# Kernel optimization log

Measured on AMD Instinct MI355X. Metric: run time of the kernel, lower is better.

Reference implementation:

```python
import jax, jax.numpy as jnp
import numpy as np

B, T, X_DIM, H, Y_DIM = 64, 2048, 256, 512, 1

def _lstm_dir(x, lens, w_ih, w_hh, b_ih, b_hh, reverse):
    # x: [B, T, In]; lens: [B] int; w_ih: [4H, In]; w_hh: [4H, H]
    Bb, Tt, _ = x.shape
    Hh = w_hh.shape[-1]
    t_idx = jnp.arange(Tt)
    if reverse:
        # reverse each sequence within its valid length (pack semantics)
        ridx = jnp.clip(lens[:, None] - 1 - t_idx[None, :], 0, Tt - 1)  # [B, T]
        x = jnp.take_along_axis(x, ridx[:, :, None], axis=1)
    valid = (t_idx[None, :] < lens[:, None]).T            # [T, B]
    xT = jnp.swapaxes(x, 0, 1)                            # [T, B, In]
    # hoist the input projection out of the scan (one big GEMM)
    x_proj = jnp.einsum('tbi,gi->tbg', xT, w_ih) + b_ih + b_hh  # [T, B, 4H]
    h0 = jnp.zeros((Bb, Hh), x.dtype)
    c0 = jnp.zeros((Bb, Hh), x.dtype)

    def step(carry, inp):
        h, c = carry
        xp, m = inp                                       # [B,4H], [B]
        g = xp + h @ w_hh.T
        i, f, gg, o = jnp.split(g, 4, axis=-1)            # torch gate order i,f,g,o
        i = jax.nn.sigmoid(i); f = jax.nn.sigmoid(f)
        gg = jnp.tanh(gg); o = jax.nn.sigmoid(o)
        c_new = f * c + i * gg
        h_new = o * jnp.tanh(c_new)
        m = m[:, None]
        h = jnp.where(m, h_new, h)                        # freeze state past seq end
        c = jnp.where(m, c_new, c)
        return (h, c), h

    (h_last, _), outs = jax.lax.scan(step, (h0, c0), (x_proj, valid))
    outs = jnp.swapaxes(outs, 0, 1)                       # [B, T, H]
    if reverse:
        ridx = jnp.clip(lens[:, None] - 1 - t_idx[None, :], 0, Tt - 1)
        outs = jnp.take_along_axis(outs, ridx[:, :, None], axis=1)
    return outs, h_last


def setup_inputs() -> dict:
    key = jax.random.key(0)
    ks = jax.random.split(key, 12)
    s = 1.0 / np.sqrt(H)
    u = lambda k, shp: jax.random.uniform(k, shp, jnp.float32, -s, s)
    seqs = jax.random.normal(ks[0], (B, T, X_DIM), jnp.float32)
    lens = jax.random.randint(ks[1], (B,), 1, T + 1)
    seqs_len = jnp.sort(lens)[::-1].astype(jnp.int64)     # descending, as pack_padded requires
    return {
        'seqs': seqs, 'seqs_len': seqs_len,
        'w_ih_l0': u(ks[2], (2, 4 * H, X_DIM)),   # [dir, 4H, in]
        'w_hh_l0': u(ks[3], (2, 4 * H, H)),
        'b_ih_l0': u(ks[4], (2, 4 * H)),
        'b_hh_l0': u(ks[5], (2, 4 * H)),
        'w_ih_l1': u(ks[6], (2, 4 * H, 2 * H)),
        'w_hh_l1': u(ks[7], (2, 4 * H, H)),
        'b_ih_l1': u(ks[8], (2, 4 * H)),
        'b_hh_l1': u(ks[9], (2, 4 * H)),
        'w_out': u(ks[10], (Y_DIM, 2 * H)),
        'b_out': u(ks[11], (Y_DIM,)),
    }


def reference(seqs, seqs_len, w_ih_l0, w_hh_l0, b_ih_l0, b_hh_l0,
              w_ih_l1, w_hh_l1, b_ih_l1, b_hh_l1, w_out, b_out):
    lens = seqs_len.astype(jnp.int32)
    x = seqs
    h_f = h_b = None
    for (wi, wh, bi, bh) in ((w_ih_l0, w_hh_l0, b_ih_l0, b_hh_l0),
                             (w_ih_l1, w_hh_l1, b_ih_l1, b_hh_l1)):
        out_f, h_f = _lstm_dir(x, lens, wi[0], wh[0], bi[0], bh[0], reverse=False)
        out_b, h_b = _lstm_dir(x, lens, wi[1], wh[1], bi[1], bh[1], reverse=True)
        x = jnp.concatenate([out_f, out_b], axis=-1)      # [B, T, 2H]
    out = jnp.concatenate([h_f, h_b], axis=1)             # last-layer final hidden, [B, 2H]
    out = jax.nn.sigmoid(out @ w_out.T + b_out)           # [B, y_dim]
    return out.squeeze(-1)                                # [B]
```

## Files before the change

### kernel.cpp

```cpp
#include <hip/hip_runtime.h>
#include <stdint.h>
#include <stddef.h>

#define B_  64
#define T_  2048
#define XD  256
#define H_  512
#define G4  2048
#define BT_ (B_*T_)

typedef __attribute__((ext_vector_type(8))) _Float16 f16x8;
typedef __attribute__((ext_vector_type(4))) float f32x4;
typedef __attribute__((ext_vector_type(4))) unsigned int u32x4;
typedef __attribute__((ext_vector_type(4))) unsigned short us4;
typedef __attribute__((ext_vector_type(2))) _Float16 f16x2;

__device__ __attribute__((aligned(256))) unsigned short g_xh[(size_t)BT_*XD];
__device__ __attribute__((aligned(256))) unsigned short g_w1h[(size_t)2*G4*XD];
__device__ __attribute__((aligned(256))) unsigned short g_w2h[(size_t)2*G4*1024];
__device__ __attribute__((aligned(256))) _Float16       g_xproj[(size_t)2*BT_*G4];
__device__ __attribute__((aligned(256))) unsigned short g_out1[(size_t)BT_*1024];
__device__ __attribute__((aligned(256))) unsigned short g_hbuf[2][2][2][B_*H_];
__device__ __attribute__((aligned(256))) float          g_hlast[2][B_*H_];
__device__ __attribute__((aligned(256))) unsigned int   g_flag[2][2][64][64];

__device__ inline unsigned short f2h(float f) {
  _Float16 h = (_Float16)f;
  return __builtin_bit_cast(unsigned short, h);
}
__device__ inline float sigf(float x)  { return 1.f/(1.f + __expf(-x)); }
__device__ inline float tanh_(float x) { return 1.f - 2.f/(__expf(2.f*x) + 1.f); }

__global__ void k_init() {
  unsigned int i = blockIdx.x*256u + threadIdx.x;
  unsigned int stride = gridDim.x*256u;
  unsigned int* hb = (unsigned int*)&g_hbuf[0][0][0][0];
  for (unsigned int j = i; j < sizeof(g_hbuf)/4; j += stride) hb[j] = 0u;
  unsigned int* fl = (unsigned int*)&g_flag[0][0][0][0];
  for (unsigned int j = i; j < sizeof(g_flag)/4; j += stride) fl[j] = 0u;
}

__global__ void k_cvt_x(const float* __restrict__ src) {
  const size_t n4 = (size_t)BT_*XD/4;
  for (size_t j = (size_t)blockIdx.x*blockDim.x + threadIdx.x; j < n4;
       j += (size_t)gridDim.x*blockDim.x) {
    float4 v = ((const float4*)src)[j];
    us4 o = { f2h(v.x), f2h(v.y), f2h(v.z), f2h(v.w) };
    ((us4*)g_xh)[j] = o;
  }
}
__global__ void k_cvt_w1(const float* __restrict__ src) {
  const size_t n4 = (size_t)2*G4*XD/4;
  for (size_t j = (size_t)blockIdx.x*blockDim.x + threadIdx.x; j < n4;
       j += (size_t)gridDim.x*blockDim.x) {
    float4 v = ((const float4*)src)[j];
    us4 o = { f2h(v.x), f2h(v.y), f2h(v.z), f2h(v.w) };
    ((us4*)g_w1h)[j] = o;
  }
}
__global__ void k_cvt_w2(const float* __restrict__ src) {
  const size_t n4 = (size_t)2*G4*1024/4;
  for (size_t j = (size_t)blockIdx.x*blockDim.x + threadIdx.x; j < n4;
       j += (size_t)gridDim.x*blockDim.x) {
    float4 v = ((const float4*)src)[j];
    us4 o = { f2h(v.x), f2h(v.y), f2h(v.z), f2h(v.w) };
    ((us4*)g_w2h)[j] = o;
  }
}

template<int LAYER>
__global__ __launch_bounds__(256) void k_xproj(const float* __restrict__ b_ih,
                                               const float* __restrict__ b_hh,
                                               const int* __restrict__ lens) {
  constexpr int K = (LAYER == 0) ? XD : 1024;
  const unsigned short* __restrict__ Abf = (LAYER == 0) ? g_xh : g_out1;
  const unsigned short* __restrict__ Wbf = (LAYER == 0) ? g_w1h : g_w2h;

  const int m0 = blockIdx.x*128;
  const int n0 = blockIdx.y*128;
  const int d  = blockIdx.z;
  const int bseq = m0 / T_;
  const int t0   = m0 % T_;
  if (t0 >= lens[bseq]) return;

  __shared__ unsigned short As[128*64];
  __shared__ unsigned short Bs[128*64];

  const int tid  = threadIdx.x;
  const int lane = tid & 63;
  const int wv   = tid >> 6;
  const int moff = (wv >> 1)*64;
  const int noff = (wv & 1)*64;

  f32x4 acc[4][4] = {};

  const unsigned short* Ag = Abf + (size_t)m0*K;
  const unsigned short* Wg = Wbf + ((size_t)d*G4 + n0)*K;

  for (int k0 = 0; k0 < K; k0 += 64) {
    __syncthreads();
    #pragma unroll
    for (int p = 0; p < 4; ++p) {
      int sidx = p*256 + tid;
      int row = sidx >> 3;
      int ch  = sidx & 7;
      u32x4 va = *(const u32x4*)(Ag + (size_t)row*K + k0 + ch*8);
      u32x4 vb = *(const u32x4*)(Wg + (size_t)row*K + k0 + ch*8);
      int wb = row*128 + ((ch ^ (row & 7)) << 4);
      *(u32x4*)((char*)As + wb) = va;
      *(u32x4*)((char*)Bs + wb) = vb;
    }
    __syncthreads();
    #pragma unroll
    for (int kt = 0; kt < 2; ++kt) {
      int slot = kt*4 + (lane >> 4);
      f16x8 af[4], bfv[4];
      #pragma unroll
      for (int mt = 0; mt < 4; ++mt) {
        int r = moff + mt*16 + (lane & 15);
        af[mt] = *(const f16x8*)((const char*)As + r*128 + ((slot ^ (r & 7)) << 4));
      }
      #pragma unroll
      for (int nt = 0; nt < 4; ++nt) {
        int r = noff + nt*16 + (lane & 15);
        bfv[nt] = *(const f16x8*)((const char*)Bs + r*128 + ((slot ^ (r & 7)) << 4));
      }
      #pragma unroll
      for (int mt = 0; mt < 4; ++mt)
        #pragma unroll
        for (int nt = 0; nt < 4; ++nt)
          acc[mt][nt] = __builtin_amdgcn_mfma_f32_16x16x32_f16(af[mt], bfv[nt], acc[mt][nt], 0, 0, 0);
    }
  }

  #pragma unroll
  for (int nt = 0; nt < 4; ++nt) {
    const int col = n0 + noff + nt*16 + (lane & 15);
    const float bias = b_ih[d*G4 + col] + b_hh[d*G4 + col];
    #pragma unroll
    for (int mt = 0; mt < 4; ++mt) {
      const int row = m0 + moff + mt*16 + (lane >> 4)*4;
      _Float16* op = g_xproj + ((size_t)d*BT_ + row)*G4 + col;
      #pragma unroll
      for (int j = 0; j < 4; ++j)
        op[(size_t)j*G4] = (_Float16)(acc[mt][nt][j] + bias);
    }
  }
}

template<int LAYER>
__global__ __launch_bounds__(256, 1) void k_scan(const float* __restrict__ w_hh,
                                                 const int* __restrict__ lens) {
  const int dir  = blockIdx.x & 1;
  const int wg   = blockIdx.x >> 1;
  const int tid  = threadIdx.x;
  const int lane = tid & 63;
  const int wv   = tid >> 6;

  __shared__ unsigned short Wl[32*512];
  __shared__ float gs[64*33];

  for (int i = tid; i < 32*256; i += 256) {
    int e = i*2;
    int row = e >> 9;
    int k   = e & 511;
    int gate = row >> 3, hc = row & 7;
    int grow = gate*H_ + wg*8 + hc;
    const float* wsrc = w_hh + ((size_t)dir*G4 + grow)*H_ + k;
    unsigned int pk = (unsigned int)f2h(wsrc[0]) | ((unsigned int)f2h(wsrc[1]) << 16);
    int byte = row*1024 + ((((k*2) >> 4) ^ (row & 7)) << 4) + ((k*2) & 15);
    *(unsigned int*)((char*)Wl + byte) = pk;
  }
  __syncthreads();

  const int myseq = tid >> 2;
  const int hcA   = (tid & 3)*2;
  const int mylen = lens[myseq];
  const int maxlen = lens[0];
  const int ml16  = __builtin_amdgcn_readfirstlane(lens[wv << 4]);
  const int col0  = wg*8;
  const int arow  = wv*16 + (lane & 15);
  const int r0f   = lane & 15, r1f = 16 + (lane & 15);
  float c0 = 0.f, c1 = 0.f, h0k = 0.f, h1k = 0.f;
  unsigned int hold = 0u;

  unsigned short* hbuf0 = &g_hbuf[LAYER][dir][0][0];
  unsigned short* hbuf1 = &g_hbuf[LAYER][dir][1][0];
  unsigned int*   flags = &g_flag[LAYER][dir][0][0];

  const unsigned int h_voff   = (unsigned int)(arow*1024 + ((lane >> 4)*16));
  const unsigned int st_voff  = (unsigned int)((myseq*H_ + col0 + hcA)*2);
  const unsigned int fan_voff = (unsigned int)(lane*256 + wg*4);
  const unsigned int pol_voff = (unsigned int)(wg*256 + lane*4);

  const char* xbase = (const char*)((const unsigned int*)
      (g_xproj + (((size_t)dir*B_ + myseq)*T_)*G4 + col0) + (hcA >> 1));

  unsigned int nx0, nx1, nx2, nx3;
  {
    int p0 = dir ? (mylen - 1) : 0;
    const char* xr = xbase + (size_t)p0*4096;
    asm volatile("global_load_dword %0, %1, off"             : "=v"(nx0) : "v"(xr) : "memory");
    asm volatile("global_load_dword %0, %1, off offset:1024" : "=v"(nx1) : "v"(xr) : "memory");
    asm volatile("global_load_dword %0, %1, off offset:2048" : "=v"(nx2) : "v"(xr) : "memory");
    asm volatile("global_load_dword %0, %1, off offset:3072" : "=v"(nx3) : "v"(xr) : "memory");
  }

  for (int s = 0; s < maxlen; ++s) {
    const unsigned short* hread = (s & 1) ? hbuf1 : hbuf0;
    unsigned short* hwrite      = (s & 1) ? hbuf0 : hbuf1;

    if (s < ml16) {
      const bool act = s < mylen;

      f16x8 aa[16];
#define HLD(I, OFS) asm volatile("global_load_dwordx4 %0, %1, %2 offset:" OFS " sc1" \
                                 : "=v"(aa[I]) : "v"(h_voff), "s"(hread) : "memory")
      HLD(0,"0");   HLD(1,"64");  HLD(2,"128"); HLD(3,"192");
      HLD(4,"256"); HLD(5,"320"); HLD(6,"384"); HLD(7,"448");
      HLD(8,"512"); HLD(9,"576"); HLD(10,"640"); HLD(11,"704");
      HLD(12,"768"); HLD(13,"832"); HLD(14,"896"); HLD(15,"960");
#undef HLD

      f16x8 b0r[16], b1r[16];
      #pragma unroll
      for (int kt = 0; kt < 16; ++kt) {
        int slot = kt*4 + (lane >> 4);
        b0r[kt] = *(const f16x8*)((const char*)Wl + r0f*1024 + ((slot ^ (r0f & 7)) << 4));
        b1r[kt] = *(const f16x8*)((const char*)Wl + r1f*1024 + ((slot ^ (r1f & 7)) << 4));
      }

      asm volatile("s_waitcnt vmcnt(0)" ::: "memory");
      __builtin_amdgcn_sched_barrier(0);
      unsigned int x0 = nx0, x1 = nx1, x2 = nx2, x3 = nx3;

      f32x4 a0e = {0.f,0.f,0.f,0.f}, a0o = {0.f,0.f,0.f,0.f};
      f32x4 a1e = {0.f,0.f,0.f,0.f}, a1o = {0.f,0.f,0.f,0.f};
      #pragma unroll
      for (int kt = 0; kt < 16; kt += 2) {
        a0e = __builtin_amdgcn_mfma_f32_16x16x32_f16(aa[kt],   b0r[kt],   a0e, 0, 0, 0);
        a1e = __builtin_amdgcn_mfma_f32_16x16x32_f16(aa[kt],   b1r[kt],   a1e, 0, 0, 0);
        a0o = __builtin_amdgcn_mfma_f32_16x16x32_f16(aa[kt+1], b0r[kt+1], a0o, 0, 0, 0);
        a1o = __builtin_amdgcn_mfma_f32_16x16x32_f16(aa[kt+1], b1r[kt+1], a1o, 0, 0, 0);
      }
      f32x4 acc0 = a0e + a0o;
      f32x4 acc1 = a1e + a1o;

      #pragma unroll
      for (int j = 0; j < 4; ++j) {
        int srow = wv*16 + (lane >> 4)*4 + j;
        gs[srow*33 + (lane & 15)]      = acc0[j];
        gs[srow*33 + 16 + (lane & 15)] = acc1[j];
      }

      {
        f16x2 p0 = __builtin_bit_cast(f16x2, x0);
        f16x2 p1 = __builtin_bit_cast(f16x2, x1);
        f16x2 p2 = __builtin_bit_cast(f16x2, x2);
        f16x2 p3 = __builtin_bit_cast(f16x2, x3);
        const int q = myseq*33;
        float vi0 = gs[q + hcA]         + (float)p0[0];
        float vi1 = gs[q + hcA + 1]     + (float)p0[1];
        float vf0 = gs[q + 8 + hcA]     + (float)p1[0];
        float vf1 = gs[q + 8 + hcA + 1] + (float)p1[1];
        float vg0 = gs[q + 16 + hcA]    + (float)p2[0];
        float vg1 = gs[q + 16 + hcA+1]  + (float)p2[1];
        float vo0 = gs[q + 24 + hcA]    + (float)p3[0];
        float vo1 = gs[q + 24 + hcA+1]  + (float)p3[1];
        if (act) {
          float i0 = sigf(vi0), f0 = sigf(vf0), G0 = tanh_(vg0), o0 = sigf(vo0);
          float i1 = sigf(vi1), f1 = sigf(vf1), G1 = tanh_(vg1), o1 = sigf(vo1);
          c0 = f0*c0 + i0*G0;
          c1 = f1*c1 + i1*G1;
          h0k = o0*tanh_(c0);
          h1k = o1*tanh_(c1);
          hold = (unsigned int)f2h(h0k) | ((unsigned int)f2h(h1k) << 16);
        }
      }

      if (s <= mylen) {
        asm volatile("global_store_dword %0, %1, %2 sc1"
                     :: "v"(st_voff), "v"(hold), "s"(hwrite) : "memory");
      }
      if (act) {
        int pos = dir ? (mylen - 1 - s) : s;
        if (LAYER == 0) {
          *(unsigned int*)(g_out1 + ((size_t)myseq*T_ + pos)*1024 + dir*H_ + col0 + hcA) = hold;
        } else {
          g_hlast[dir][myseq*H_ + col0 + hcA]     = h0k;
          g_hlast[dir][myseq*H_ + col0 + hcA + 1] = h1k;
        }
      }

      {
        int s1 = s + 1;
        int p1 = dir ? (mylen - 1 - s1) : s1;
        p1 = p1 < 0 ? 0 : (p1 > mylen - 1 ? mylen - 1 : p1);
        const char* xr = xbase + (size_t)p1*4096;
        asm volatile("global_load_dword %0, %1, off"             : "=v"(nx0) : "v"(xr) : "memory");
        asm volatile("global_load_dword %0, %1, off offset:1024" : "=v"(nx1) : "v"(xr) : "memory");
        asm volatile("global_load_dword %0, %1, off offset:2048" : "=v"(nx2) : "v"(xr) : "memory");
        asm volatile("global_load_dword %0, %1, off offset:3072" : "=v"(nx3) : "v"(xr) : "memory");
      }

      asm volatile("s_waitcnt vmcnt(4)" ::: "memory");
    }

    asm volatile("s_barrier" ::: "memory");
    if (wv == 0) {
      unsigned int fv = (unsigned int)(s + 1);
      asm volatile("global_store_dword %0, %1, %2 sc1"
                   :: "v"(fan_voff), "v"(fv), "s"(flags) : "memory");
      const unsigned int tgt = fv;
      while (true) {
        unsigned int v;
        asm volatile("global_load_dword %0, %1, %2 sc1"
                     : "=v"(v) : "v"(pol_voff), "s"(flags) : "memory");
        asm volatile("s_waitcnt vmcnt(0)" ::: "memory");
        if (__all(v >= tgt)) break;
        __builtin_amdgcn_s_sleep(1);
      }
    }
    asm volatile("s_barrier" ::: "memory");
  }
}

__global__ void k_final(const float* __restrict__ w_out, const float* __restrict__ b_out,
                        float* __restrict__ out) {
  const int b = blockIdx.x;
  const int tid = threadIdx.x;
  float sum = 0.f;
  for (int k = tid; k < 1024; k += 256) {
    float h = (k < 512) ? g_hlast[0][b*H_ + k] : g_hlast[1][b*H_ + k - 512];
    sum += h * w_out[k];
  }
  __shared__ float red[256];
  red[tid] = sum;
  __syncthreads();
  for (int st = 128; st > 0; st >>= 1) {
    if (tid < st) red[tid] += red[tid + st];
    __syncthreads();
  }
  if (tid == 0) out[b] = 1.f/(1.f + __expf(-(red[0] + b_out[0])));
}

extern "C" void kernel_launch(void* const* d_in, const int* in_sizes, int n_in,
                              void* d_out, int out_size, void* d_ws, size_t ws_size,
                              hipStream_t stream) {
  (void)in_sizes; (void)n_in; (void)d_ws; (void)ws_size; (void)out_size;
  const float* seqs    = (const float*)d_in[0];
  const int*   lens    = (const int*)d_in[1];
  const float* w_ih_l0 = (const float*)d_in[2];
  const float* w_hh_l0 = (const float*)d_in[3];
  const float* b_ih_l0 = (const float*)d_in[4];
  const float* b_hh_l0 = (const float*)d_in[5];
  const float* w_ih_l1 = (const float*)d_in[6];
  const float* w_hh_l1 = (const float*)d_in[7];
  const float* b_ih_l1 = (const float*)d_in[8];
  const float* b_hh_l1 = (const float*)d_in[9];
  const float* w_out   = (const float*)d_in[10];
  const float* b_out   = (const float*)d_in[11];
  float* outp = (float*)d_out;

  hipLaunchKernelGGL(k_init,   dim3(256),  dim3(256), 0, stream);
  hipLaunchKernelGGL(k_cvt_x,  dim3(2048), dim3(256), 0, stream, seqs);
  hipLaunchKernelGGL(k_cvt_w1, dim3(256),  dim3(256), 0, stream, w_ih_l0);
  hipLaunchKernelGGL(k_cvt_w2, dim3(512),  dim3(256), 0, stream, w_ih_l1);

  hipLaunchKernelGGL((k_xproj<0>), dim3(BT_/128, 16, 2), dim3(256), 0, stream,
                     b_ih_l0, b_hh_l0, lens);
  {
    void* args[] = { (void*)&w_hh_l0, (void*)&lens };
    hipError_t e = hipLaunchCooperativeKernel(k_scan<0>, dim3(128), dim3(256), args, 0u, stream);
    (void)e;
  }
  hipLaunchKernelGGL((k_xproj<1>), dim3(BT_/128, 16, 2), dim3(256), 0, stream,
                     b_ih_l1, b_hh_l1, lens);
  {
    void* args[] = { (void*)&w_hh_l1, (void*)&lens };
    hipError_t e = hipLaunchCooperativeKernel(k_scan<1>, dim3(128), dim3(256), args, 0u, stream);
    (void)e;
  }
  hipLaunchKernelGGL(k_final, dim3(64), dim3(256), 0, stream, w_out, b_out, outp);
}
```

Before: 17.11 ms.

## Replace all-to-all flag barrier with gather-then-broadcast grid barrier

The per-timestep cross-workgroup barrier in the persistent LSTM recurrence used an all-to-all flag matrix: each workgroup wrote its flag to every peer's slot and polled 64 flags. Now each workgroup writes one owner flag, workgroup 0 gathers all 64 and then publishes a single broadcast word that the other workgroups poll. This cuts the stores and the polled cache lines per step. In exchange it adds a serial hop through workgroup 0, which lengthens the barrier's critical path, and all workgroups now contend on one polled line.

```diff
diff --git a/kernel.cpp b/kernel.cpp
--- a/kernel.cpp
+++ b/kernel.cpp
@@ -22,7 +22,8 @@
 __device__ __attribute__((aligned(256))) unsigned short g_out1[(size_t)BT_*1024];
 __device__ __attribute__((aligned(256))) unsigned short g_hbuf[2][2][2][B_*H_];
 __device__ __attribute__((aligned(256))) float          g_hlast[2][B_*H_];
-__device__ __attribute__((aligned(256))) unsigned int   g_flag[2][2][64][64];
+__device__ __attribute__((aligned(256))) unsigned int   g_ownf[2][2][64][32];
+__device__ __attribute__((aligned(256))) unsigned int   g_bcast[2][2][32];
 
 __device__ inline unsigned short f2h(float f) {
   _Float16 h = (_Float16)f;
@@ -36,8 +37,10 @@
   unsigned int stride = gridDim.x*256u;
   unsigned int* hb = (unsigned int*)&g_hbuf[0][0][0][0];
   for (unsigned int j = i; j < sizeof(g_hbuf)/4; j += stride) hb[j] = 0u;
-  unsigned int* fl = (unsigned int*)&g_flag[0][0][0][0];
-  for (unsigned int j = i; j < sizeof(g_flag)/4; j += stride) fl[j] = 0u;
+  unsigned int* fl = (unsigned int*)&g_ownf[0][0][0][0];
+  for (unsigned int j = i; j < sizeof(g_ownf)/4; j += stride) fl[j] = 0u;
+  unsigned int* bc = (unsigned int*)&g_bcast[0][0][0];
+  for (unsigned int j = i; j < sizeof(g_bcast)/4; j += stride) bc[j] = 0u;
 }
 
 __global__ void k_cvt_x(const float* __restrict__ src) {
@@ -186,12 +189,13 @@
 
   unsigned short* hbuf0 = &g_hbuf[LAYER][dir][0][0];
   unsigned short* hbuf1 = &g_hbuf[LAYER][dir][1][0];
-  unsigned int*   flags = &g_flag[LAYER][dir][0][0];
+  unsigned int*   ownf  = &g_ownf[LAYER][dir][0][0];
+  unsigned int*   bc    = &g_bcast[LAYER][dir][0];
 
   const unsigned int h_voff   = (unsigned int)(arow*1024 + ((lane >> 4)*16));
   const unsigned int st_voff  = (unsigned int)((myseq*H_ + col0 + hcA)*2);
-  const unsigned int fan_voff = (unsigned int)(lane*256 + wg*4);
-  const unsigned int pol_voff = (unsigned int)(wg*256 + lane*4);
+  const unsigned int own_voff = (unsigned int)(wg*128);
+  const unsigned int gat_voff = (unsigned int)(lane*128);
 
   const char* xbase = (const char*)((const unsigned int*)
       (g_xproj + (((size_t)dir*B_ + myseq)*T_)*G4 + col0) + (hcA >> 1));
@@ -307,15 +311,31 @@
     }
 
     asm volatile("s_barrier" ::: "memory");
-    if (wv == 0) {
-      unsigned int fv = (unsigned int)(s + 1);
+    const unsigned int tgt = (unsigned int)(s + 1);
+    if (tid == 0) {
       asm volatile("global_store_dword %0, %1, %2 sc1"
-                   :: "v"(fan_voff), "v"(fv), "s"(flags) : "memory");
-      const unsigned int tgt = fv;
+                   :: "v"(own_voff), "v"(tgt), "s"(ownf) : "memory");
+    }
+    if (wg == 0) {
+      if (wv == 0) {
+        while (true) {
+          unsigned int v;
+          asm volatile("global_load_dword %0, %1, %2 sc1"
+                       : "=v"(v) : "v"(gat_voff), "s"(ownf) : "memory");
+          asm volatile("s_waitcnt vmcnt(0)" ::: "memory");
+          if (__all(v >= tgt)) break;
+          __builtin_amdgcn_s_sleep(1);
+        }
+        if (lane == 0) {
+          asm volatile("global_store_dword %0, %1, %2 sc1"
+                       :: "v"(0u), "v"(tgt), "s"(bc) : "memory");
+        }
+      }
+    } else if (wv == 0) {
       while (true) {
         unsigned int v;
         asm volatile("global_load_dword %0, %1, %2 sc1"
-                     : "=v"(v) : "v"(pol_voff), "s"(flags) : "memory");
+                     : "=v"(v) : "v"(0u), "s"(bc) : "memory");
         asm volatile("s_waitcnt vmcnt(0)" ::: "memory");
         if (__all(v >= tgt)) break;
         __builtin_amdgcn_s_sleep(1);
```

Measured after the change: 17.62 ms. 1.03x slower.

## Halve scan workgroups, give each 16 hidden columns to cut barrier participants

Applied to the files above, without the earlier changes.

The recurrent scan now uses 32 workgroups per direction instead of 64. Each workgroup owns 16 hidden columns (64 weight rows in LDS), runs four MFMA accumulators per step, and each thread updates four cells with vectorized loads and stores. The grid-wide flag barrier now polls 32 flags, which shortens the per-step synchronization. In exchange, each workgroup does twice the per-step MFMA and gate work on the critical path, and the weight fragments are read from LDS inside the MFMA loop instead of being held in registers. The layer-1 final hidden state is also written once after the loop rather than on every step.

```diff
diff --git a/kernel.cpp b/kernel.cpp
--- a/kernel.cpp
+++ b/kernel.cpp
@@ -10,10 +10,11 @@
 #define BT_ (B_*T_)
 
 typedef __attribute__((ext_vector_type(8))) _Float16 f16x8;
+typedef __attribute__((ext_vector_type(4))) _Float16 f16x4;
 typedef __attribute__((ext_vector_type(4))) float f32x4;
 typedef __attribute__((ext_vector_type(4))) unsigned int u32x4;
+typedef __attribute__((ext_vector_type(2))) unsigned int u32x2;
 typedef __attribute__((ext_vector_type(4))) unsigned short us4;
-typedef __attribute__((ext_vector_type(2))) _Float16 f16x2;
 
 __device__ __attribute__((aligned(256))) unsigned short g_xh[(size_t)BT_*XD];
 __device__ __attribute__((aligned(256))) unsigned short g_w1h[(size_t)2*G4*XD];
@@ -22,7 +23,7 @@
 __device__ __attribute__((aligned(256))) unsigned short g_out1[(size_t)BT_*1024];
 __device__ __attribute__((aligned(256))) unsigned short g_hbuf[2][2][2][B_*H_];
 __device__ __attribute__((aligned(256))) float          g_hlast[2][B_*H_];
-__device__ __attribute__((aligned(256))) unsigned int   g_flag[2][2][64][64];
+__device__ __attribute__((aligned(256))) unsigned int   g_flag[2][2][32][32];
 
 __device__ inline unsigned short f2h(float f) {
   _Float16 h = (_Float16)f;
@@ -157,15 +158,15 @@
   const int lane = tid & 63;
   const int wv   = tid >> 6;
 
-  __shared__ unsigned short Wl[32*512];
-  __shared__ float gs[64*33];
-
-  for (int i = tid; i < 32*256; i += 256) {
+  __shared__ unsigned short Wl[64*512];
+  __shared__ float gs[64*65];
+
+  for (int i = tid; i < 64*256; i += 256) {
     int e = i*2;
     int row = e >> 9;
     int k   = e & 511;
-    int gate = row >> 3, hc = row & 7;
-    int grow = gate*H_ + wg*8 + hc;
+    int gate = row >> 4, hc = row & 15;
+    int grow = gate*H_ + wg*16 + hc;
     const float* wsrc = w_hh + ((size_t)dir*G4 + grow)*H_ + k;
     unsigned int pk = (unsigned int)f2h(wsrc[0]) | ((unsigned int)f2h(wsrc[1]) << 16);
     int byte = row*1024 + ((((k*2) >> 4) ^ (row & 7)) << 4) + ((k*2) & 15);
@@ -174,15 +175,16 @@
   __syncthreads();
 
   const int myseq = tid >> 2;
-  const int hcA   = (tid & 3)*2;
+  const int hcA   = (tid & 3)*4;
   const int mylen = lens[myseq];
   const int maxlen = lens[0];
   const int ml16  = __builtin_amdgcn_readfirstlane(lens[wv << 4]);
-  const int col0  = wg*8;
+  const int col0  = wg*16;
   const int arow  = wv*16 + (lane & 15);
-  const int r0f   = lane & 15, r1f = 16 + (lane & 15);
-  float c0 = 0.f, c1 = 0.f, h0k = 0.f, h1k = 0.f;
-  unsigned int hold = 0u;
+  const int r0f = lane & 15, r1f = 16 + (lane & 15), r2f = 32 + (lane & 15), r3f = 48 + (lane & 15);
+  float c0 = 0.f, c1 = 0.f, c2 = 0.f, c3 = 0.f;
+  float h0k = 0.f, h1k = 0.f, h2k = 0.f, h3k = 0.f;
+  u32x2 hold = {0u, 0u};
 
   unsigned short* hbuf0 = &g_hbuf[LAYER][dir][0][0];
   unsigned short* hbuf1 = &g_hbuf[LAYER][dir][1][0];
@@ -190,20 +192,20 @@
 
   const unsigned int h_voff   = (unsigned int)(arow*1024 + ((lane >> 4)*16));
   const unsigned int st_voff  = (unsigned int)((myseq*H_ + col0 + hcA)*2);
-  const unsigned int fan_voff = (unsigned int)(lane*256 + wg*4);
-  const unsigned int pol_voff = (unsigned int)(wg*256 + lane*4);
-
-  const char* xbase = (const char*)((const unsigned int*)
-      (g_xproj + (((size_t)dir*B_ + myseq)*T_)*G4 + col0) + (hcA >> 1));
-
-  unsigned int nx0, nx1, nx2, nx3;
+  const unsigned int fan_voff = (unsigned int)(lane*128 + wg*4);
+  const unsigned int pol_voff = (unsigned int)(wg*128 + (lane & 31)*4);
+
+  const char* xbase = (const char*)
+      (g_xproj + (((size_t)dir*B_ + myseq)*T_)*G4 + col0 + hcA);
+
+  u32x2 nx0, nx1, nx2, nx3;
   {
     int p0 = dir ? (mylen - 1) : 0;
     const char* xr = xbase + (size_t)p0*4096;
-    asm volatile("global_load_dword %0, %1, off"             : "=v"(nx0) : "v"(xr) : "memory");
-    asm volatile("global_load_dword %0, %1, off offset:1024" : "=v"(nx1) : "v"(xr) : "memory");
-    asm volatile("global_load_dword %0, %1, off offset:2048" : "=v"(nx2) : "v"(xr) : "memory");
-    asm volatile("global_load_dword %0, %1, off offset:3072" : "=v"(nx3) : "v"(xr) : "memory");
+    asm volatile("global_load_dwordx2 %0, %1, off"             : "=v"(nx0) : "v"(xr) : "memory");
+    asm volatile("global_load_dwordx2 %0, %1, off offset:1024" : "=v"(nx1) : "v"(xr) : "memory");
+    asm volatile("global_load_dwordx2 %0, %1, off offset:2048" : "=v"(nx2) : "v"(xr) : "memory");
+    asm volatile("global_load_dwordx2 %0, %1, off offset:3072" : "=v"(nx3) : "v"(xr) : "memory");
   }
 
   for (int s = 0; s < maxlen; ++s) {
@@ -222,73 +224,70 @@
       HLD(12,"768"); HLD(13,"832"); HLD(14,"896"); HLD(15,"960");
 #undef HLD
 
-      f16x8 b0r[16], b1r[16];
+      asm volatile("s_waitcnt vmcnt(0)" ::: "memory");
+      __builtin_amdgcn_sched_barrier(0);
+      u32x2 x0 = nx0, x1 = nx1, x2 = nx2, x3 = nx3;
+
+      f32x4 acc0 = {0.f,0.f,0.f,0.f};
+      f32x4 acc1 = {0.f,0.f,0.f,0.f};
+      f32x4 acc2 = {0.f,0.f,0.f,0.f};
+      f32x4 acc3 = {0.f,0.f,0.f,0.f};
       #pragma unroll
       for (int kt = 0; kt < 16; ++kt) {
         int slot = kt*4 + (lane >> 4);
-        b0r[kt] = *(const f16x8*)((const char*)Wl + r0f*1024 + ((slot ^ (r0f & 7)) << 4));
-        b1r[kt] = *(const f16x8*)((const char*)Wl + r1f*1024 + ((slot ^ (r1f & 7)) << 4));
-      }
-
-      asm volatile("s_waitcnt vmcnt(0)" ::: "memory");
-      __builtin_amdgcn_sched_barrier(0);
-      unsigned int x0 = nx0, x1 = nx1, x2 = nx2, x3 = nx3;
-
-      f32x4 a0e = {0.f,0.f,0.f,0.f}, a0o = {0.f,0.f,0.f,0.f};
-      f32x4 a1e = {0.f,0.f,0.f,0.f}, a1o = {0.f,0.f,0.f,0.f};
-      #pragma unroll
-      for (int kt = 0; kt < 16; kt += 2) {
-        a0e = __builtin_amdgcn_mfma_f32_16x16x32_f16(aa[kt],   b0r[kt],   a0e, 0, 0, 0);
-        a1e = __builtin_amdgcn_mfma_f32_16x16x32_f16(aa[kt],   b1r[kt],   a1e, 0, 0, 0);
-        a0o = __builtin_amdgcn_mfma_f32_16x16x32_f16(aa[kt+1], b0r[kt+1], a0o, 0, 0, 0);
-        a1o = __builtin_amdgcn_mfma_f32_16x16x32_f16(aa[kt+1], b1r[kt+1], a1o, 0, 0, 0);
-      }
-      f32x4 acc0 = a0e + a0o;
-      f32x4 acc1 = a1e + a1o;
+        f16x8 b0 = *(const f16x8*)((const char*)Wl + r0f*1024 + ((slot ^ (r0f & 7)) << 4));
+        f16x8 b1 = *(const f16x8*)((const char*)Wl + r1f*1024 + ((slot ^ (r1f & 7)) << 4));
+        f16x8 b2 = *(const f16x8*)((const char*)Wl + r2f*1024 + ((slot ^ (r2f & 7)) << 4));
+        f16x8 b3 = *(const f16x8*)((const char*)Wl + r3f*1024 + ((slot ^ (r3f & 7)) << 4));
+        acc0 = __builtin_amdgcn_mfma_f32_16x16x32_f16(aa[kt], b0, acc0, 0, 0, 0);
+        acc1 = __builtin_amdgcn_mfma_f32_16x16x32_f16(aa[kt], b1, acc1, 0, 0, 0);
+        acc2 = __builtin_amdgcn_mfma_f32_16x16x32_f16(aa[kt], b2, acc2, 0, 0, 0);
+        acc3 = __builtin_amdgcn_mfma_f32_16x16x32_f16(aa[kt], b3, acc3, 0, 0, 0);
+      }
 
       #pragma unroll
       for (int j = 0; j < 4; ++j) {
         int srow = wv*16 + (lane >> 4)*4 + j;
-        gs[srow*33 + (lane & 15)]      = acc0[j];
-        gs[srow*33 + 16 + (lane & 15)] = acc1[j];
+        gs[srow*65 +      (lane & 15)] = acc0[j];
+        gs[srow*65 + 16 + (lane & 15)] = acc1[j];
+        gs[srow*65 + 32 + (lane & 15)] = acc2[j];
+        gs[srow*65 + 48 + (lane & 15)] = acc3[j];
       }
 
       {
-        f16x2 p0 = __builtin_bit_cast(f16x2, x0);
-        f16x2 p1 = __builtin_bit_cast(f16x2, x1);
-        f16x2 p2 = __builtin_bit_cast(f16x2, x2);
-        f16x2 p3 = __builtin_bit_cast(f16x2, x3);
-        const int q = myseq*33;
-        float vi0 = gs[q + hcA]         + (float)p0[0];
-        float vi1 = gs[q + hcA + 1]     + (float)p0[1];
-        float vf0 = gs[q + 8 + hcA]     + (float)p1[0];
-        float vf1 = gs[q + 8 + hcA + 1] + (float)p1[1];
-        float vg0 = gs[q + 16 + hcA]    + (float)p2[0];
-        float vg1 = gs[q + 16 + hcA+1]  + (float)p2[1];
-        float vo0 = gs[q + 24 + hcA]    + (float)p3[0];
-        float vo1 = gs[q + 24 + hcA+1]  + (float)p3[1];
+        f16x4 pi = __builtin_bit_cast(f16x4, x0);
+        f16x4 pf = __builtin_bit_cast(f16x4, x1);
+        f16x4 pg = __builtin_bit_cast(f16x4, x2);
+        f16x4 po = __builtin_bit_cast(f16x4, x3);
+        const int q = myseq*65;
         if (act) {
-          float i0 = sigf(vi0), f0 = sigf(vf0), G0 = tanh_(vg0), o0 = sigf(vo0);
-          float i1 = sigf(vi1), f1 = sigf(vf1), G1 = tanh_(vg1), o1 = sigf(vo1);
-          c0 = f0*c0 + i0*G0;
-          c1 = f1*c1 + i1*G1;
-          h0k = o0*tanh_(c0);
-          h1k = o1*tanh_(c1);
-          hold = (unsigned int)f2h(h0k) | ((unsigned int)f2h(h1k) << 16);
+          float cc[4] = {c0, c1, c2, c3};
+          float hh[4];
+          #pragma unroll
+          for (int t = 0; t < 4; ++t) {
+            float vi = gs[q +      hcA + t] + (float)pi[t];
+            float vf = gs[q + 16 + hcA + t] + (float)pf[t];
+            float vg = gs[q + 32 + hcA + t] + (float)pg[t];
+            float vo = gs[q + 48 + hcA + t] + (float)po[t];
+            float ig = sigf(vi), fg = sigf(vf), gg = tanh_(vg), og = sigf(vo);
+            cc[t] = fg*cc[t] + ig*gg;
+            hh[t] = og*tanh_(cc[t]);
+          }
+          c0 = cc[0]; c1 = cc[1]; c2 = cc[2]; c3 = cc[3];
+          h0k = hh[0]; h1k = hh[1]; h2k = hh[2]; h3k = hh[3];
+          hold.x = (unsigned int)f2h(h0k) | ((unsigned int)f2h(h1k) << 16);
+          hold.y = (unsigned int)f2h(h2k) | ((unsigned int)f2h(h3k) << 16);
         }
       }
 
       if (s <= mylen) {
-        asm volatile("global_store_dword %0, %1, %2 sc1"
+        asm volatile("global_store_dwordx2 %0, %1, %2 sc1"
                      :: "v"(st_voff), "v"(hold), "s"(hwrite) : "memory");
       }
-      if (act) {
-        int pos = dir ? (mylen - 1 - s) : s;
-        if (LAYER == 0) {
-          *(unsigned int*)(g_out1 + ((size_t)myseq*T_ + pos)*1024 + dir*H_ + col0 + hcA) = hold;
-        } else {
-          g_hlast[dir][myseq*H_ + col0 + hcA]     = h0k;
-          g_hlast[dir][myseq*H_ + col0 + hcA + 1] = h1k;
+      if (LAYER == 0) {
+        if (s < mylen) {
+          int pos = dir ? (mylen - 1 - s) : s;
+          *(u32x2*)(g_out1 + ((size_t)myseq*T_ + pos)*1024 + dir*H_ + col0 + hcA) = hold;
         }
       }
 
@@ -297,20 +296,23 @@
         int p1 = dir ? (mylen - 1 - s1) : s1;
         p1 = p1 < 0 ? 0 : (p1 > mylen - 1 ? mylen - 1 : p1);
         const char* xr = xbase + (size_t)p1*4096;
-        asm volatile("global_load_dword %0, %1, off"             : "=v"(nx0) : "v"(xr) : "memory");
-        asm volatile("global_load_dword %0, %1, off offset:1024" : "=v"(nx1) : "v"(xr) : "memory");
-        asm volatile("global_load_dword %0, %1, off offset:2048" : "=v"(nx2) : "v"(xr) : "memory");
-        asm volatile("global_load_dword %0, %1, off offset:3072" : "=v"(nx3) : "v"(xr) : "memory");
-      }
-
-      asm volatile("s_waitcnt vmcnt(4)" ::: "memory");
+        asm volatile("global_load_dwordx2 %0, %1, off"             : "=v"(nx0) : "v"(xr) : "memory");
+        asm volatile("global_load_dwordx2 %0, %1, off offset:1024" : "=v"(nx1) : "v"(xr) : "memory");
+        asm volatile("global_load_dwordx2 %0, %1, off offset:2048" : "=v"(nx2) : "v"(xr) : "memory");
+        asm volatile("global_load_dwordx2 %0, %1, off offset:3072" : "=v"(nx3) : "v"(xr) : "memory");
+      }
+
+      if (LAYER == 0) asm volatile("s_waitcnt vmcnt(5)" ::: "memory");
+      else            asm volatile("s_waitcnt vmcnt(4)" ::: "memory");
     }
 
     asm volatile("s_barrier" ::: "memory");
     if (wv == 0) {
       unsigned int fv = (unsigned int)(s + 1);
-      asm volatile("global_store_dword %0, %1, %2 sc1"
-                   :: "v"(fan_voff), "v"(fv), "s"(flags) : "memory");
+      if (lane < 32) {
+        asm volatile("global_store_dword %0, %1, %2 sc1"
+                     :: "v"(fan_voff), "v"(fv), "s"(flags) : "memory");
+      }
       const unsigned int tgt = fv;
       while (true) {
         unsigned int v;
@@ -322,6 +324,13 @@
       }
     }
     asm volatile("s_barrier" ::: "memory");
+  }
+
+  if (LAYER == 1) {
+    g_hlast[dir][myseq*H_ + col0 + hcA]     = h0k;
+    g_hlast[dir][myseq*H_ + col0 + hcA + 1] = h1k;
+    g_hlast[dir][myseq*H_ + col0 + hcA + 2] = h2k;
+    g_hlast[dir][myseq*H_ + col0 + hcA + 3] = h3k;
   }
 }
 
@@ -371,14 +380,14 @@
                      b_ih_l0, b_hh_l0, lens);
   {
     void* args[] = { (void*)&w_hh_l0, (void*)&lens };
-    hipError_t e = hipLaunchCooperativeKernel(k_scan<0>, dim3(128), dim3(256), args, 0u, stream);
+    hipError_t e = hipLaunchCooperativeKernel(k_scan<0>, dim3(64), dim3(256), args, 0u, stream);
     (void)e;
   }
   hipLaunchKernelGGL((k_xproj<1>), dim3(BT_/128, 16, 2), dim3(256), 0, stream,
                      b_ih_l1, b_hh_l1, lens);
   {
     void* args[] = { (void*)&w_hh_l1, (void*)&lens };
-    hipError_t e = hipLaunchCooperativeKernel(k_scan<1>, dim3(128), dim3(256), args, 0u, stream);
+    hipError_t e = hipLaunchCooperativeKernel(k_scan<1>, dim3(64), dim3(256), args, 0u, stream);
     (void)e;
   }
   hipLaunchKernelGGL(k_final, dim3(64), dim3(256), 0, stream, w_out, b_out, outp);
```

New measurement: 20.91 ms. +22.2%, slower.

## Replace flag barrier with per-step tagged h exchange; use direct LDS loads in GEMM

Applied to the files above, without the earlier changes.

The recurrent kernel drops the separate flag array and the per-step cross-workgroup barrier. Each hidden-state dword is now stored next to a step tag in a triple-buffered global array, and readers spin until every tag matches the current step, so synchronisation becomes dataflow rather than a global barrier. The input-projection GEMM now uses global_load_lds direct-to-LDS copies without the XOR swizzle and remaps block order across M. The tags double the traffic on the h exchange, and the unswizzled LDS layout may add bank conflicts.

```diff
diff --git a/kernel.cpp b/kernel.cpp
--- a/kernel.cpp
+++ b/kernel.cpp
@@ -15,14 +15,16 @@
 typedef __attribute__((ext_vector_type(4))) unsigned short us4;
 typedef __attribute__((ext_vector_type(2))) _Float16 f16x2;
 
+typedef __attribute__((address_space(3))) unsigned short lds_us;
+typedef __attribute__((address_space(1))) const unsigned short gl_us;
+
 __device__ __attribute__((aligned(256))) unsigned short g_xh[(size_t)BT_*XD];
 __device__ __attribute__((aligned(256))) unsigned short g_w1h[(size_t)2*G4*XD];
 __device__ __attribute__((aligned(256))) unsigned short g_w2h[(size_t)2*G4*1024];
 __device__ __attribute__((aligned(256))) _Float16       g_xproj[(size_t)2*BT_*G4];
 __device__ __attribute__((aligned(256))) unsigned short g_out1[(size_t)BT_*1024];
-__device__ __attribute__((aligned(256))) unsigned short g_hbuf[2][2][2][B_*H_];
 __device__ __attribute__((aligned(256))) float          g_hlast[2][B_*H_];
-__device__ __attribute__((aligned(256))) unsigned int   g_flag[2][2][64][64];
+__device__ __attribute__((aligned(256))) unsigned int   g_hx[2][2][3][B_][128][4];
 
 __device__ inline unsigned short f2h(float f) {
   _Float16 h = (_Float16)f;
@@ -34,10 +36,8 @@
 __global__ void k_init() {
   unsigned int i = blockIdx.x*256u + threadIdx.x;
   unsigned int stride = gridDim.x*256u;
-  unsigned int* hb = (unsigned int*)&g_hbuf[0][0][0][0];
-  for (unsigned int j = i; j < sizeof(g_hbuf)/4; j += stride) hb[j] = 0u;
-  unsigned int* fl = (unsigned int*)&g_flag[0][0][0][0];
-  for (unsigned int j = i; j < sizeof(g_flag)/4; j += stride) fl[j] = 0u;
+  unsigned int* hx = (unsigned int*)&g_hx[0][0][0][0][0][0];
+  for (unsigned int j = i; j < sizeof(g_hx)/4; j += stride) hx[j] = 0u;
 }
 
 __global__ void k_cvt_x(const float* __restrict__ src) {
@@ -76,7 +76,9 @@
   const unsigned short* __restrict__ Abf = (LAYER == 0) ? g_xh : g_out1;
   const unsigned short* __restrict__ Wbf = (LAYER == 0) ? g_w1h : g_w2h;
 
-  const int m0 = blockIdx.x*128;
+  const int nmx = gridDim.x;
+  const int bx  = (int)((blockIdx.x & 7)*(nmx >> 3) + (blockIdx.x >> 3));
+  const int m0 = bx*128;
   const int n0 = blockIdx.y*128;
   const int d  = blockIdx.z;
   const int bseq = m0 / T_;
@@ -97,18 +99,19 @@
   const unsigned short* Ag = Abf + (size_t)m0*K;
   const unsigned short* Wg = Wbf + ((size_t)d*G4 + n0)*K;
 
+  const int srow_l = lane >> 3;
+  const int scol_l = (lane & 7)*8;
+
   for (int k0 = 0; k0 < K; k0 += 64) {
     __syncthreads();
     #pragma unroll
-    for (int p = 0; p < 4; ++p) {
-      int sidx = p*256 + tid;
-      int row = sidx >> 3;
-      int ch  = sidx & 7;
-      u32x4 va = *(const u32x4*)(Ag + (size_t)row*K + k0 + ch*8);
-      u32x4 vb = *(const u32x4*)(Wg + (size_t)row*K + k0 + ch*8);
-      int wb = row*128 + ((ch ^ (row & 7)) << 4);
-      *(u32x4*)((char*)As + wb) = va;
-      *(u32x4*)((char*)Bs + wb) = vb;
+    for (int j = 0; j < 4; ++j) {
+      const int inst = wv*4 + j;
+      const int row  = inst*8 + srow_l;
+      const unsigned short* ga = Ag + (size_t)row*K + k0 + scol_l;
+      const unsigned short* gb = Wg + (size_t)row*K + k0 + scol_l;
+      __builtin_amdgcn_global_load_lds((gl_us*)ga, (lds_us*)(As + inst*512), 16, 0, 0);
+      __builtin_amdgcn_global_load_lds((gl_us*)gb, (lds_us*)(Bs + inst*512), 16, 0, 0);
     }
     __syncthreads();
     #pragma unroll
@@ -118,12 +121,12 @@
       #pragma unroll
       for (int mt = 0; mt < 4; ++mt) {
         int r = moff + mt*16 + (lane & 15);
-        af[mt] = *(const f16x8*)((const char*)As + r*128 + ((slot ^ (r & 7)) << 4));
+        af[mt] = *(const f16x8*)(As + r*64 + slot*8);
       }
       #pragma unroll
       for (int nt = 0; nt < 4; ++nt) {
         int r = noff + nt*16 + (lane & 15);
-        bfv[nt] = *(const f16x8*)((const char*)Bs + r*128 + ((slot ^ (r & 7)) << 4));
+        bfv[nt] = *(const f16x8*)(Bs + r*64 + slot*8);
       }
       #pragma unroll
       for (int mt = 0; mt < 4; ++mt)
@@ -176,22 +179,21 @@
   const int myseq = tid >> 2;
   const int hcA   = (tid & 3)*2;
   const int mylen = lens[myseq];
-  const int maxlen = lens[0];
   const int ml16  = __builtin_amdgcn_readfirstlane(lens[wv << 4]);
   const int col0  = wg*8;
   const int arow  = wv*16 + (lane & 15);
+  const int lenA  = lens[arow];
+  const int half  = lane >> 4;
   const int r0f   = lane & 15, r1f = 16 + (lane & 15);
   float c0 = 0.f, c1 = 0.f, h0k = 0.f, h1k = 0.f;
   unsigned int hold = 0u;
 
-  unsigned short* hbuf0 = &g_hbuf[LAYER][dir][0][0];
-  unsigned short* hbuf1 = &g_hbuf[LAYER][dir][1][0];
-  unsigned int*   flags = &g_flag[LAYER][dir][0][0];
-
-  const unsigned int h_voff   = (unsigned int)(arow*1024 + ((lane >> 4)*16));
-  const unsigned int st_voff  = (unsigned int)((myseq*H_ + col0 + hcA)*2);
-  const unsigned int fan_voff = (unsigned int)(lane*256 + wg*4);
-  const unsigned int pol_voff = (unsigned int)(wg*256 + lane*4);
+  const unsigned int* hxbase = &g_hx[LAYER][dir][0][0][0][0];
+  const unsigned int BUFB = 64*128*16;
+
+  const unsigned int rd_base = (unsigned int)(arow*2048 + half*32);
+  const unsigned int wr_base = (unsigned int)(myseq*2048 + (wg*2 + ((tid & 3) >> 1))*16);
+  const bool is_writer = (tid & 1) == 0;
 
   const char* xbase = (const char*)((const unsigned int*)
       (g_xproj + (((size_t)dir*B_ + myseq)*T_)*G4 + col0) + (hcA >> 1));
@@ -206,122 +208,126 @@
     asm volatile("global_load_dword %0, %1, off offset:3072" : "=v"(nx3) : "v"(xr) : "memory");
   }
 
-  for (int s = 0; s < maxlen; ++s) {
-    const unsigned short* hread = (s & 1) ? hbuf1 : hbuf0;
-    unsigned short* hwrite      = (s & 1) ? hbuf0 : hbuf1;
-
-    if (s < ml16) {
-      const bool act = s < mylen;
-
-      f16x8 aa[16];
-#define HLD(I, OFS) asm volatile("global_load_dwordx4 %0, %1, %2 offset:" OFS " sc1" \
-                                 : "=v"(aa[I]) : "v"(h_voff), "s"(hread) : "memory")
-      HLD(0,"0");   HLD(1,"64");  HLD(2,"128"); HLD(3,"192");
-      HLD(4,"256"); HLD(5,"320"); HLD(6,"384"); HLD(7,"448");
-      HLD(8,"512"); HLD(9,"576"); HLD(10,"640"); HLD(11,"704");
-      HLD(12,"768"); HLD(13,"832"); HLD(14,"896"); HLD(15,"960");
-#undef HLD
-
-      f16x8 b0r[16], b1r[16];
-      #pragma unroll
-      for (int kt = 0; kt < 16; ++kt) {
-        int slot = kt*4 + (lane >> 4);
-        b0r[kt] = *(const f16x8*)((const char*)Wl + r0f*1024 + ((slot ^ (r0f & 7)) << 4));
-        b1r[kt] = *(const f16x8*)((const char*)Wl + r1f*1024 + ((slot ^ (r1f & 7)) << 4));
-      }
-
+  int rb = 0;
+  for (int s = 0; s < ml16; ++s) {
+    const int wb = (rb == 2) ? 0 : rb + 1;
+    const unsigned int rd_voff = (unsigned int)rb*BUFB + rd_base;
+    const unsigned int wr_voff = (unsigned int)wb*BUFB + wr_base;
+    const bool act = s < mylen;
+    const unsigned int tgt = (unsigned int)s;
+    const bool staleok = (s >= lenA);
+
+    u32x4 g[32];
+    while (true) {
+#define GLD(I, OFS) asm volatile("global_load_dwordx4 %0, %1, %2 offset:" OFS " sc1" \
+                                 : "=v"(g[I]) : "v"(rd_voff), "s"(hxbase) : "memory")
+      GLD(0,"0");    GLD(1,"16");   GLD(2,"128");  GLD(3,"144");
+      GLD(4,"256");  GLD(5,"272");  GLD(6,"384");  GLD(7,"400");
+      GLD(8,"512");  GLD(9,"528");  GLD(10,"640"); GLD(11,"656");
+      GLD(12,"768"); GLD(13,"784"); GLD(14,"896"); GLD(15,"912");
+      GLD(16,"1024");GLD(17,"1040");GLD(18,"1152");GLD(19,"1168");
+      GLD(20,"1280");GLD(21,"1296");GLD(22,"1408");GLD(23,"1424");
+      GLD(24,"1536");GLD(25,"1552");GLD(26,"1664");GLD(27,"1680");
+      GLD(28,"1792");GLD(29,"1808");GLD(30,"1920");GLD(31,"1936");
+#undef GLD
       asm volatile("s_waitcnt vmcnt(0)" ::: "memory");
       __builtin_amdgcn_sched_barrier(0);
-      unsigned int x0 = nx0, x1 = nx1, x2 = nx2, x3 = nx3;
-
-      f32x4 a0e = {0.f,0.f,0.f,0.f}, a0o = {0.f,0.f,0.f,0.f};
-      f32x4 a1e = {0.f,0.f,0.f,0.f}, a1o = {0.f,0.f,0.f,0.f};
-      #pragma unroll
-      for (int kt = 0; kt < 16; kt += 2) {
-        a0e = __builtin_amdgcn_mfma_f32_16x16x32_f16(aa[kt],   b0r[kt],   a0e, 0, 0, 0);
-        a1e = __builtin_amdgcn_mfma_f32_16x16x32_f16(aa[kt],   b1r[kt],   a1e, 0, 0, 0);
-        a0o = __builtin_amdgcn_mfma_f32_16x16x32_f16(aa[kt+1], b0r[kt+1], a0o, 0, 0, 0);
-        a1o = __builtin_amdgcn_mfma_f32_16x16x32_f16(aa[kt+1], b1r[kt+1], a1o, 0, 0, 0);
-      }
-      f32x4 acc0 = a0e + a0o;
-      f32x4 acc1 = a1e + a1o;
-
-      #pragma unroll
-      for (int j = 0; j < 4; ++j) {
-        int srow = wv*16 + (lane >> 4)*4 + j;
-        gs[srow*33 + (lane & 15)]      = acc0[j];
-        gs[srow*33 + 16 + (lane & 15)] = acc1[j];
-      }
-
-      {
-        f16x2 p0 = __builtin_bit_cast(f16x2, x0);
-        f16x2 p1 = __builtin_bit_cast(f16x2, x1);
-        f16x2 p2 = __builtin_bit_cast(f16x2, x2);
-        f16x2 p3 = __builtin_bit_cast(f16x2, x3);
-        const int q = myseq*33;
-        float vi0 = gs[q + hcA]         + (float)p0[0];
-        float vi1 = gs[q + hcA + 1]     + (float)p0[1];
-        float vf0 = gs[q + 8 + hcA]     + (float)p1[0];
-        float vf1 = gs[q + 8 + hcA + 1] + (float)p1[1];
-        float vg0 = gs[q + 16 + hcA]    + (float)p2[0];
-        float vg1 = gs[q + 16 + hcA+1]  + (float)p2[1];
-        float vo0 = gs[q + 24 + hcA]    + (float)p3[0];
-        float vo1 = gs[q + 24 + hcA+1]  + (float)p3[1];
-        if (act) {
-          float i0 = sigf(vi0), f0 = sigf(vf0), G0 = tanh_(vg0), o0 = sigf(vo0);
-          float i1 = sigf(vi1), f1 = sigf(vf1), G1 = tanh_(vg1), o1 = sigf(vo1);
-          c0 = f0*c0 + i0*G0;
-          c1 = f1*c1 + i1*G1;
-          h0k = o0*tanh_(c0);
-          h1k = o1*tanh_(c1);
-          hold = (unsigned int)f2h(h0k) | ((unsigned int)f2h(h1k) << 16);
-        }
-      }
-
-      if (s <= mylen) {
-        asm volatile("global_store_dword %0, %1, %2 sc1"
-                     :: "v"(st_voff), "v"(hold), "s"(hwrite) : "memory");
-      }
+      bool ok = staleok;
+      if (!ok) {
+        ok = true;
+        #pragma unroll
+        for (int i = 0; i < 32; ++i)
+          ok = ok && (g[i].y == tgt) && (g[i].w == tgt);
+      }
+      if (__all(ok)) break;
+      __builtin_amdgcn_s_sleep(1);
+    }
+    __builtin_amdgcn_sched_barrier(0);
+    unsigned int x0 = nx0, x1 = nx1, x2 = nx2, x3 = nx3;
+
+    f32x4 a0e = {0.f,0.f,0.f,0.f}, a0o = {0.f,0.f,0.f,0.f};
+    f32x4 a1e = {0.f,0.f,0.f,0.f}, a1o = {0.f,0.f,0.f,0.f};
+    #pragma unroll
+    for (int kt = 0; kt < 16; kt += 2) {
+      u32x4 t0v = { g[2*kt].x,   g[2*kt].z,   g[2*kt+1].x, g[2*kt+1].z };
+      u32x4 t1v = { g[2*kt+2].x, g[2*kt+2].z, g[2*kt+3].x, g[2*kt+3].z };
+      f16x8 aE = __builtin_bit_cast(f16x8, t0v);
+      f16x8 aO = __builtin_bit_cast(f16x8, t1v);
+      int sl0 = kt*4 + half, sl1 = (kt+1)*4 + half;
+      f16x8 b0a = *(const f16x8*)((const char*)Wl + r0f*1024 + ((sl0 ^ (r0f & 7)) << 4));
+      f16x8 b1a = *(const f16x8*)((const char*)Wl + r1f*1024 + ((sl0 ^ (r1f & 7)) << 4));
+      f16x8 b0b = *(const f16x8*)((const char*)Wl + r0f*1024 + ((sl1 ^ (r0f & 7)) << 4));
+      f16x8 b1b = *(const f16x8*)((const char*)Wl + r1f*1024 + ((sl1 ^ (r1f & 7)) << 4));
+      a0e = __builtin_amdgcn_mfma_f32_16x16x32_f16(aE, b0a, a0e, 0, 0, 0);
+      a1e = __builtin_amdgcn_mfma_f32_16x16x32_f16(aE, b1a, a1e, 0, 0, 0);
+      a0o = __builtin_amdgcn_mfma_f32_16x16x32_f16(aO, b0b, a0o, 0, 0, 0);
+      a1o = __builtin_amdgcn_mfma_f32_16x16x32_f16(aO, b1b, a1o, 0, 0, 0);
+    }
+    f32x4 acc0 = a0e + a0o;
+    f32x4 acc1 = a1e + a1o;
+
+    #pragma unroll
+    for (int j = 0; j < 4; ++j) {
+      int srow = wv*16 + (lane >> 4)*4 + j;
+      gs[srow*33 + (lane & 15)]      = acc0[j];
+      gs[srow*33 + 16 + (lane & 15)] = acc1[j];
+    }
+
+    {
+      f16x2 p0 = __builtin_bit_cast(f16x2, x0);
+      f16x2 p1 = __builtin_bit_cast(f16x2, x1);
+      f16x2 p2 = __builtin_bit_cast(f16x2, x2);
+      f16x2 p3 = __builtin_bit_cast(f16x2, x3);
+      const int q = myseq*33;
+      float vi0 = gs[q + hcA]         + (float)p0[0];
+      float vi1 = gs[q + hcA + 1]     + (float)p0[1];
+      float vf0 = gs[q + 8 + hcA]     + (float)p1[0];
+      float vf1 = gs[q + 8 + hcA + 1] + (float)p1[1];
+      float vg0 = gs[q + 16 + hcA]    + (float)p2[0];
+      float vg1 = gs[q + 16 + hcA+1]  + (float)p2[1];
+      float vo0 = gs[q + 24 + hcA]    + (float)p3[0];
+      float vo1 = gs[q + 24 + hcA+1]  + (float)p3[1];
+      if (act) {
+        float i0 = sigf(vi0), f0 = sigf(vf0), G0 = tanh_(vg0), o0 = sigf(vo0);
+        float i1 = sigf(vi1), f1 = sigf(vf1), G1 = tanh_(vg1), o1 = sigf(vo1);
+        c0 = f0*c0 + i0*G0;
+        c1 = f1*c1 + i1*G1;
+        h0k = o0*tanh_(c0);
+        h1k = o1*tanh_(c1);
+        hold = (unsigned int)f2h(h0k) | ((unsigned int)f2h(h1k) << 16);
+      }
+    }
+
+    unsigned int hp = __shfl_xor(hold, 1);
+    if (is_writer && act) {
+      u32x4 st = { hold, (unsigned int)(s + 1), hp, (unsigned int)(s + 1) };
+      asm volatile("global_store_dwordx4 %0, %1, %2 sc1"
+                   :: "v"(wr_voff), "v"(st), "s"(hxbase) : "memory");
+    }
+    if (LAYER == 0) {
       if (act) {
         int pos = dir ? (mylen - 1 - s) : s;
-        if (LAYER == 0) {
-          *(unsigned int*)(g_out1 + ((size_t)myseq*T_ + pos)*1024 + dir*H_ + col0 + hcA) = hold;
-        } else {
-          g_hlast[dir][myseq*H_ + col0 + hcA]     = h0k;
-          g_hlast[dir][myseq*H_ + col0 + hcA + 1] = h1k;
-        }
-      }
-
-      {
-        int s1 = s + 1;
-        int p1 = dir ? (mylen - 1 - s1) : s1;
-        p1 = p1 < 0 ? 0 : (p1 > mylen - 1 ? mylen - 1 : p1);
-        const char* xr = xbase + (size_t)p1*4096;
-        asm volatile("global_load_dword %0, %1, off"             : "=v"(nx0) : "v"(xr) : "memory");
-        asm volatile("global_load_dword %0, %1, off offset:1024" : "=v"(nx1) : "v"(xr) : "memory");
-        asm volatile("global_load_dword %0, %1, off offset:2048" : "=v"(nx2) : "v"(xr) : "memory");
-        asm volatile("global_load_dword %0, %1, off offset:3072" : "=v"(nx3) : "v"(xr) : "memory");
-      }
-
-      asm volatile("s_waitcnt vmcnt(4)" ::: "memory");
-    }
-
-    asm volatile("s_barrier" ::: "memory");
-    if (wv == 0) {
-      unsigned int fv = (unsigned int)(s + 1);
-      asm volatile("global_store_dword %0, %1, %2 sc1"
-                   :: "v"(fan_voff), "v"(fv), "s"(flags) : "memory");
-      const unsigned int tgt = fv;
-      while (true) {
-        unsigned int v;
-        asm volatile("global_load_dword %0, %1, %2 sc1"
-                     : "=v"(v) : "v"(pol_voff), "s"(flags) : "memory");
-        asm volatile("s_waitcnt vmcnt(0)" ::: "memory");
-        if (__all(v >= tgt)) break;
-        __builtin_amdgcn_s_sleep(1);
-      }
-    }
-    asm volatile("s_barrier" ::: "memory");
+        *(unsigned int*)(g_out1 + ((size_t)myseq*T_ + pos)*1024 + dir*H_ + col0 + hcA) = hold;
+      }
+    }
+
+    {
+      int s1 = s + 1;
+      int p1 = dir ? (mylen - 1 - s1) : s1;
+      p1 = p1 < 0 ? 0 : (p1 > mylen - 1 ? mylen - 1 : p1);
+      const char* xr = xbase + (size_t)p1*4096;
+      asm volatile("global_load_dword %0, %1, off"             : "=v"(nx0) : "v"(xr) : "memory");
+      asm volatile("global_load_dword %0, %1, off offset:1024" : "=v"(nx1) : "v"(xr) : "memory");
+      asm volatile("global_load_dword %0, %1, off offset:2048" : "=v"(nx2) : "v"(xr) : "memory");
+      asm volatile("global_load_dword %0, %1, off offset:3072" : "=v"(nx3) : "v"(xr) : "memory");
+    }
+
+    rb = wb;
+  }
+
+  if (LAYER == 1) {
+    g_hlast[dir][myseq*H_ + col0 + hcA]     = h0k;
+    g_hlast[dir][myseq*H_ + col0 + hcA + 1] = h1k;
   }
 }
 
```

Result: slower. 27.76 ms (+62.2%).
